# Performance work log

Measured on AMD Instinct MI355X. Metric: run time of the kernel, lower is better.

## Reference

```python
import jax, jax.numpy as jnp
import numpy as np

N_NODES = 100000
N_EDGES = 1600000
D = 64
N_GRAPHS = 64


def setup_inputs() -> dict:
    key = jax.random.key(0)
    ks = jax.random.split(key, 12)
    x = jax.random.normal(ks[0], (N_NODES, D), dtype=jnp.float32)
    edge_index = jax.random.randint(ks[1], (2, N_EDGES), 0, N_NODES, dtype=jnp.int32)
    batch = jnp.sort(jax.random.randint(ks[2], (N_NODES,), 0, N_GRAPHS, dtype=jnp.int32))
    s = 1.0 / np.sqrt(D)
    W1 = jax.random.uniform(ks[3], (D, D), jnp.float32, -s, s)
    b1 = jax.random.uniform(ks[4], (D,), jnp.float32, -s, s)
    W2 = jax.random.uniform(ks[5], (D, D), jnp.float32, -s, s)
    b2 = jax.random.uniform(ks[6], (D,), jnp.float32, -s, s)
    W3 = jax.random.uniform(ks[7], (D, D), jnp.float32, -s, s)
    b3 = jax.random.uniform(ks[8], (D,), jnp.float32, -s, s)
    lin_w = jax.random.uniform(ks[9], (D, 1), jnp.float32, -s, s)
    lin_b = jax.random.uniform(ks[10], (1,), jnp.float32, -s, s)
    return {"x": x, "edge_index": edge_index, "batch": batch,
            "W1": W1, "b1": b1, "W2": W2, "b2": b2, "W3": W3, "b3": b3,
            "lin_w": lin_w, "lin_b": lin_b}


def _gcn_conv(x, src, dst, norm, W, b):
    # PyG GCNConv: linear first, then normalized gather-scatter aggregation.
    h = x @ W                                   # [N, D]
    msg = h[src] * norm[:, None]                # [E+N, D] gathered + scaled
    out = jax.ops.segment_sum(msg, dst, num_segments=N_NODES)
    return out + b


def reference(x, edge_index, batch, W1, b1, W2, b2, W3, b3, lin_w, lin_b):
    loops = jnp.arange(N_NODES, dtype=edge_index.dtype)
    src = jnp.concatenate([edge_index[0], loops])  # source j
    dst = jnp.concatenate([edge_index[1], loops])  # target i
    # symmetric normalization D^{-1/2}(A+I)D^{-1/2}; deg >= 1 due to self loops
    deg = jax.ops.segment_sum(jnp.ones_like(dst, dtype=x.dtype), dst, num_segments=N_NODES)
    dis = jax.lax.rsqrt(deg)
    norm = dis[src] * dis[dst]                  # per-edge scalar
    h = jax.nn.relu(_gcn_conv(x, src, dst, norm, W1, b1))
    h = jax.nn.relu(_gcn_conv(h, src, dst, norm, W2, b2))
    h = jax.nn.relu(_gcn_conv(h, src, dst, norm, W3, b3))
    pooled = jax.ops.segment_sum(h, batch, num_segments=N_GRAPHS)  # global_add_pool
    return pooled @ lin_w + lin_b               # [N_GRAPHS, 1]
```

## Files before the change

kernel.cpp:

```cpp
#include <hip/hip_runtime.h>
#include <hip/hip_fp16.h>

#define D 64
#define NBMAX 512
#define BCAP 5120
#define TILE 64
#define AST 68
#define ACAP 448

typedef __attribute__((ext_vector_type(8))) short short8;
typedef __attribute__((ext_vector_type(4))) float float4v;

static __device__ __forceinline__ unsigned short f2bf(float x) {
    unsigned u = __float_as_uint(x);
    u += 0x7FFFu + ((u >> 16) & 1);
    return (unsigned short)(u >> 16);
}

__global__ void zero_ints(int* __restrict__ p, int n) {
    int i = blockIdx.x * blockDim.x + threadIdx.x;
    if (i < n) p[i] = 0;
}

__global__ void prescale_x(const float* __restrict__ x, const float* __restrict__ dis,
                           __half* __restrict__ out, int n2) {
    int i = blockIdx.x * blockDim.x + threadIdx.x;
    if (i < n2) {
        int n = i >> 5;
        float d = dis[n];
        float2 v = ((const float2*)x)[i];
        ((__half2*)out)[i] = __floats2half2_rn(v.x * d, v.y * d);
    }
}

__global__ __launch_bounds__(256) void bucket_scatter(const int* __restrict__ src,
                                                      const int* __restrict__ dst, int E,
                                                      int nb, int* __restrict__ gcursor,
                                                      unsigned* __restrict__ bpair) {
    __shared__ int lhist[NBMAX];
    __shared__ int lbase[NBMAX];
    int t = threadIdx.x;
    for (int i = t; i < nb; i += 256) lhist[i] = 0;
    __syncthreads();
    int e0 = blockIdx.x * 4096, e1 = min(e0 + 4096, E);
    for (int e = e0 + t; e < e1; e += 256) atomicAdd(&lhist[dst[e] >> 8], 1);
    __syncthreads();
    for (int i = t; i < nb; i += 256) {
        int c = lhist[i];
        lbase[i] = c ? atomicAdd(&gcursor[i], c) : 0;
        lhist[i] = 0;
    }
    __syncthreads();
    for (int e = e0 + t; e < e1; e += 256) {
        int d = dst[e];
        int b = d >> 8;
        int r = lbase[b] + atomicAdd(&lhist[b], 1);
        if (r < BCAP)
            bpair[(long)b * BCAP + r] = ((unsigned)src[e] << 8) | (unsigned)(d & 255);
    }
}

__global__ void scan_buckets(const int* __restrict__ gcursor, int B, int* __restrict__ gbase) {
    __shared__ int s[512];
    int t = threadIdx.x;
    s[t] = (t < B) ? gcursor[t] : 0;
    __syncthreads();
    for (int off = 1; off < 512; off <<= 1) {
        int v = (t >= off) ? s[t - off] : 0;
        __syncthreads();
        s[t] += v;
        __syncthreads();
    }
    if (t < B) gbase[t] = (t == 0) ? 0 : s[t - 1];
    if (t == 0) gbase[B] = s[511];
}

__global__ __launch_bounds__(256) void bucket_build(const unsigned* __restrict__ bpair,
                                                    int nb, int N,
                                                    const int* __restrict__ gcursor,
                                                    const int* __restrict__ gbase,
                                                    int* __restrict__ row_ptr,
                                                    float* __restrict__ dis,
                                                    int* __restrict__ adj) {
    __shared__ int hist[256];
    __shared__ int cur[256];
    __shared__ int wsum[4];
    int b = blockIdx.x, t = threadIdx.x;
    int cnt = gcursor[b];
    if (cnt > BCAP) cnt = BCAP;
    int ebase = gbase[b];
    const unsigned* bp = bpair + (long)b * BCAP;

    hist[t] = 0;
    __syncthreads();
    for (int i = t; i < cnt; i += 256) atomicAdd(&hist[bp[i] & 255u], 1);
    __syncthreads();
    int val = hist[t];
    int lane = t & 63, wv = t >> 6;
    int v = val;
#pragma unroll
    for (int off = 1; off < 64; off <<= 1) {
        int u = __shfl_up(v, off, 64);
        if (lane >= off) v += u;
    }
    if (lane == 63) wsum[wv] = v;
    __syncthreads();
    int wo = 0;
#pragma unroll
    for (int w = 0; w < 4; w++)
        if (w < wv) wo += wsum[w];
    int excl = wo + v - val;
    int node = (b << 8) + t;
    if (node < N) {
        row_ptr[node] = ebase + excl;
        dis[node] = rsqrtf((float)(val + 1));
    }
    cur[t] = ebase + excl;
    __syncthreads();
    for (int i = t; i < cnt; i += 256) {
        unsigned p = bp[i];
        unsigned dl = p & 255u;
        int pos = atomicAdd(&cur[dl], 1);
        adj[pos] = (int)((p >> 8) << 6) | (int)(dl & 63u);
    }
    if (b == 0 && t == 0) row_ptr[N] = gbase[nb];
}

__global__ __launch_bounds__(256) void tile_layer(const __half* __restrict__ in,
                                                  const int* __restrict__ row_ptr,
                                                  const int* __restrict__ adj,
                                                  const float* __restrict__ dis,
                                                  const float* __restrict__ Wg,
                                                  const float* __restrict__ bias,
                                                  __half* __restrict__ out,
                                                  int N, int scale_out) {
    __shared__ float acc[TILE * AST];
    __shared__ int adjbuf[4][ACAP];

    int t = threadIdx.x;
    int lane = t & 63;
    int w = t >> 6;
    int row = lane >> 2;
    int c = lane & 3;
    int c2 = c * 2;
    int col = lane & 15, quad = lane >> 4;

    int t0 = blockIdx.x * TILE;
    int wbase = t0 + w * 16;
    int node = wbase + row;

    int e0r = 0, e1r = 0;
    if (node < N) { e0r = row_ptr[node]; e1r = row_ptr[node + 1]; }

    const int4* in4 = (const int4*)in;
    int* adjw = adjbuf[w];

    float a[16];
#pragma unroll
    for (int j = 0; j < 16; j++) a[j] = 0.f;

#define ADD16(xa, ya)                                                   \
    {                                                                   \
        const __half2* h0 = (const __half2*)&(xa);                      \
        const __half2* h1 = (const __half2*)&(ya);                      \
        _Pragma("unroll")                                               \
        for (int j = 0; j < 4; j++) {                                   \
            float2 f = __half22float2(h0[j]);                           \
            a[2 * j] += f.x; a[2 * j + 1] += f.y;                       \
        }                                                               \
        _Pragma("unroll")                                               \
        for (int j = 0; j < 4; j++) {                                   \
            float2 f = __half22float2(h1[j]);                           \
            a[8 + 2 * j] += f.x; a[8 + 2 * j + 1] += f.y;               \
        }                                                               \
    }

    if (node < N) {
        long rs = (long)node * 8 + c2;
        int4 xa = in4[rs], xb = in4[rs + 1];
        ADD16(xa, xb)
    }

    int wn0 = min(wbase, N);
    int wn1 = min(wbase + 16, N);
    int eb_w = row_ptr[wn0];
    int ee_w = row_ptr[wn1];

    for (int base = eb_w; base < ee_w; base += ACAP) {
        int clen = min(ACAP, ee_w - base);
        for (int i = lane; i < clen; i += 64) adjw[i] = adj[base + i];
        __builtin_amdgcn_s_waitcnt(0);

        int ls = max(e0r - base, 0);
        int le = min(e1r - base, clen);
        int cnt = max(le - ls, 0);
        int kmax = cnt;
#pragma unroll
        for (int off = 32; off >= 1; off >>= 1) {
            int o = __shfl_xor(kmax, off, 64);
            kmax = max(kmax, o);
        }
        int sidx = min(ls, clen - 1);

        for (int k = 0; k < kmax; k += 4) {
            int i0 = ls + k;
            bool ok0 = i0 < le, ok1 = i0 + 1 < le, ok2 = i0 + 2 < le, ok3 = i0 + 3 < le;
            int p0 = adjw[ok0 ? i0 : sidx];
            int p1 = adjw[ok1 ? i0 + 1 : sidx];
            int p2 = adjw[ok2 ? i0 + 2 : sidx];
            int p3 = adjw[ok3 ? i0 + 3 : sidx];
            long r0 = (long)(p0 >> 6) * 8 + c2;
            long r1 = (long)(p1 >> 6) * 8 + c2;
            long r2 = (long)(p2 >> 6) * 8 + c2;
            long r3 = (long)(p3 >> 6) * 8 + c2;
            int4 xa0 = in4[r0], xb0 = in4[r0 + 1];
            int4 xa1 = in4[r1], xb1 = in4[r1 + 1];
            int4 xa2 = in4[r2], xb2 = in4[r2 + 1];
            int4 xa3 = in4[r3], xb3 = in4[r3 + 1];
            if (ok0) ADD16(xa0, xb0)
            if (ok1) ADD16(xa1, xb1)
            if (ok2) ADD16(xa2, xb2)
            if (ok3) ADD16(xa3, xb3)
        }
    }
#undef ADD16

    int nl = w * 16 + row;
    float* ap_out = &acc[nl * AST + c * 16];
#pragma unroll
    for (int j = 0; j < 4; j++) {
        float4v v4 = {a[4 * j], a[4 * j + 1], a[4 * j + 2], a[4 * j + 3]};
        *(float4v*)(ap_out + 4 * j) = v4;
    }
    __builtin_amdgcn_s_waitcnt(0);

    short8 Bf[2][4];
#pragma unroll
    for (int s = 0; s < 2; s++)
#pragma unroll
        for (int cc = 0; cc < 4; cc++) {
            short8 f;
#pragma unroll
            for (int j = 0; j < 8; j++)
                f[j] = (short)f2bf(Wg[(32 * s + quad * 8 + j) * D + 16 * cc + col]);
            Bf[s][cc] = f;
        }
    float bias_c[4];
#pragma unroll
    for (int cc = 0; cc < 4; cc++) bias_c[cc] = bias[16 * cc + col];

    int arow = w * 16 + col;
    int anode = t0 + arow;
    float dA = (anode < N) ? dis[anode] : 0.f;
    short8 Af[2];
#pragma unroll
    for (int s = 0; s < 2; s++) {
        const float* ap = &acc[arow * AST + 32 * s + quad * 8];
        float4v p0 = *(const float4v*)ap;
        float4v p1 = *(const float4v*)(ap + 4);
        short8 f;
#pragma unroll
        for (int j = 0; j < 4; j++) {
            f[j] = (short)f2bf(p0[j] * dA);
            f[4 + j] = (short)f2bf(p1[j] * dA);
        }
        Af[s] = f;
    }

    float4v accv[4];
#pragma unroll
    for (int cc = 0; cc < 4; cc++) {
        float4v z = {0.f, 0.f, 0.f, 0.f};
        accv[cc] = __builtin_amdgcn_mfma_f32_16x16x32_bf16(Af[0], Bf[0][cc], z, 0, 0, 0);
        accv[cc] = __builtin_amdgcn_mfma_f32_16x16x32_bf16(Af[1], Bf[1][cc], accv[cc], 0, 0, 0);
    }

#pragma unroll
    for (int r = 0; r < 4; r++) {
        int onode = t0 + w * 16 + quad * 4 + r;
        if (onode < N) {
            float dn = scale_out ? dis[onode] : 1.f;
#pragma unroll
            for (int cc = 0; cc < 4; cc++) {
                float vv = fmaxf(accv[cc][r] + bias_c[cc], 0.f) * dn;
                out[(long)onode * D + 16 * cc + col] = __float2half(vv);
            }
        }
    }
}

__global__ __launch_bounds__(256) void pool_partial(const __half* __restrict__ h,
                                                    const int* __restrict__ batch, int N,
                                                    int chunk, float* __restrict__ pooled) {
    int lane = threadIdx.x & 63;
    int wv = threadIdx.x >> 6;
    int c0 = blockIdx.x * chunk;
    int c1 = min(c0 + chunk, N);
    int g_cur = -1;
    float acc = 0.f;
    for (int n = c0 + wv; n < c1; n += 4) {
        int g = batch[n];
        if (g != g_cur) {
            if (g_cur >= 0) atomicAdd(&pooled[g_cur * D + lane], acc);
            g_cur = g;
            acc = 0.f;
        }
        acc += __half2float(h[n * D + lane]);
    }
    if (g_cur >= 0) atomicAdd(&pooled[g_cur * D + lane], acc);
}

__global__ void pool_linear(const float* __restrict__ pooled,
                            const float* __restrict__ lin_w,
                            const float* __restrict__ lin_b,
                            float* __restrict__ out, int G) {
    int lane = threadIdx.x & 63;
    int g = blockIdx.x * (blockDim.x >> 6) + (threadIdx.x >> 6);
    if (g >= G) return;
    float t = pooled[g * D + lane] * lin_w[lane];
#pragma unroll
    for (int off = 32; off >= 1; off >>= 1) t += __shfl_down(t, off, 64);
    if (lane == 0) out[g] = t + lin_b[0];
}

extern "C" void kernel_launch(void* const* d_in, const int* in_sizes, int n_in,
                              void* d_out, int out_size, void* d_ws, size_t ws_size,
                              hipStream_t stream) {
    const float* x      = (const float*)d_in[0];
    const int*   edges  = (const int*)d_in[1];
    const int*   batch  = (const int*)d_in[2];
    const float* W1     = (const float*)d_in[3];
    const float* b1     = (const float*)d_in[4];
    const float* W2     = (const float*)d_in[5];
    const float* b2     = (const float*)d_in[6];
    const float* W3     = (const float*)d_in[7];
    const float* b3     = (const float*)d_in[8];
    const float* lin_w  = (const float*)d_in[9];
    const float* lin_b  = (const float*)d_in[10];
    float* out = (float*)d_out;

    const int N = in_sizes[2];
    const int E = in_sizes[1] / 2;
    const int G = out_size;
    const int nb = (N + 255) >> 8;

    const int* e_src = edges;
    const int* e_dst = edges + E;

    auto al = [](long v) { return (v + 63) & ~63L; };
    long o_gcur   = 0;
    long o_pooled = al(o_gcur + NBMAX);
    long o_gbase  = al(o_pooled + (long)G * D);
    long o_rowptr = al(o_gbase + nb + 1);
    long o_dis    = al(o_rowptr + N + 1);
    long o_adjs   = al(o_dis + N);
    long o_xh     = al(o_adjs + E);
    long o_hA     = al(o_xh + (long)N * D / 2);
    long o_hB     = o_hA + (long)N * D;

    int*    gcursor = (int*)d_ws + o_gcur;
    float*  pooled  = (float*)d_ws + o_pooled;
    int*    gbase   = (int*)d_ws + o_gbase;
    int*    row_ptr = (int*)d_ws + o_rowptr;
    float*  dis     = (float*)d_ws + o_dis;
    int*    adj     = (int*)d_ws + o_adjs;
    __half* xh      = (__half*)((float*)d_ws + o_xh);
    __half* hA      = (__half*)((float*)d_ws + o_hA);
    __half* hB      = (__half*)((float*)d_ws + o_hB);
    unsigned* bpair = (unsigned*)hA;

    int nz = (int)(o_pooled + (long)G * D);
    zero_ints<<<(nz + 255) / 256, 256, 0, stream>>>((int*)d_ws, nz);

    bucket_scatter<<<(E + 4095) / 4096, 256, 0, stream>>>(e_src, e_dst, E, nb, gcursor, bpair);
    scan_buckets<<<1, 512, 0, stream>>>(gcursor, nb, gbase);
    bucket_build<<<nb, 256, 0, stream>>>(bpair, nb, N, gcursor, gbase, row_ptr, dis, adj);

    int n2 = N * D / 2;
    prescale_x<<<(n2 + 255) / 256, 256, 0, stream>>>(x, dis, xh, n2);

    const int tl_blocks = (N + TILE - 1) / TILE;
    tile_layer<<<tl_blocks, 256, 0, stream>>>(xh, row_ptr, adj, dis, W1, b1, hB, N, 1);
    tile_layer<<<tl_blocks, 256, 0, stream>>>(hB, row_ptr, adj, dis, W2, b2, hA, N, 1);
    tile_layer<<<tl_blocks, 256, 0, stream>>>(hA, row_ptr, adj, dis, W3, b3, hB, N, 0);

    const int pool_blocks = 512;
    const int chunk = (N + pool_blocks - 1) / pool_blocks;
    pool_partial<<<pool_blocks, 256, 0, stream>>>(hB, batch, N, chunk, pooled);
    pool_linear<<<(G + 3) / 4, 256, 0, stream>>>(pooled, lin_w, lin_b, out, G);
}
```

Before: 277.6 us.

## Shrink tile_layer registers and LDS: bf16 staging, templated gather unroll, streamed weights

Turns the GCN tile layer into a template over the gather batch size. Layer 1 keeps a 4-wide gather; layers 2 and 3 use a 2-wide gather with launch_bounds(256,8) to raise occupancy. The aggregated rows are now scaled by dis and packed to bf16 before going to LDS, which halves shared memory use. Weight fragments are loaded per column block instead of all up front, and the index math uses 32-bit byte offsets. Fewer gathers in flight per wave on layers 2 and 3 could reduce memory-level parallelism, and forcing 8 blocks per CU may cause register spills.

```diff
diff --git a/kernel.cpp b/kernel.cpp
--- a/kernel.cpp
+++ b/kernel.cpp
@@ -5,7 +5,7 @@
 #define NBMAX 512
 #define BCAP 5120
 #define TILE 64
-#define AST 68
+#define ASTH 72
 #define ACAP 448
 
 typedef __attribute__((ext_vector_type(8))) short short8;
@@ -126,15 +126,16 @@
     if (b == 0 && t == 0) row_ptr[N] = gbase[nb];
 }
 
-__global__ __launch_bounds__(256) void tile_layer(const __half* __restrict__ in,
-                                                  const int* __restrict__ row_ptr,
-                                                  const int* __restrict__ adj,
-                                                  const float* __restrict__ dis,
-                                                  const float* __restrict__ Wg,
-                                                  const float* __restrict__ bias,
-                                                  __half* __restrict__ out,
-                                                  int N, int scale_out) {
-    __shared__ float acc[TILE * AST];
+template <int NB>
+static __device__ __forceinline__ void tile_layer_body(const __half* __restrict__ in,
+                                                       const int* __restrict__ row_ptr,
+                                                       const int* __restrict__ adj,
+                                                       const float* __restrict__ dis,
+                                                       const float* __restrict__ Wg,
+                                                       const float* __restrict__ bias,
+                                                       __half* __restrict__ out,
+                                                       int N, int scale_out) {
+    __shared__ __align__(16) unsigned short accb[TILE * ASTH];
     __shared__ int adjbuf[4][ACAP];
 
     int t = threadIdx.x;
@@ -142,7 +143,6 @@
     int w = t >> 6;
     int row = lane >> 2;
     int c = lane & 3;
-    int c2 = c * 2;
     int col = lane & 15, quad = lane >> 4;
 
     int t0 = blockIdx.x * TILE;
@@ -152,8 +152,9 @@
     int e0r = 0, e1r = 0;
     if (node < N) { e0r = row_ptr[node]; e1r = row_ptr[node + 1]; }
 
-    const int4* in4 = (const int4*)in;
+    const char* inb = (const char*)in;
     int* adjw = adjbuf[w];
+    unsigned coff = (unsigned)c * 32u;
 
     float a[16];
 #pragma unroll
@@ -176,8 +177,9 @@
     }
 
     if (node < N) {
-        long rs = (long)node * 8 + c2;
-        int4 xa = in4[rs], xb = in4[rs + 1];
+        unsigned rb = (unsigned)node * 128u + coff;
+        int4 xa = *(const int4*)(inb + rb);
+        int4 xb = *(const int4*)(inb + rb + 16);
         ADD16(xa, xb)
     }
 
@@ -202,91 +204,93 @@
         }
         int sidx = min(ls, clen - 1);
 
-        for (int k = 0; k < kmax; k += 4) {
-            int i0 = ls + k;
-            bool ok0 = i0 < le, ok1 = i0 + 1 < le, ok2 = i0 + 2 < le, ok3 = i0 + 3 < le;
-            int p0 = adjw[ok0 ? i0 : sidx];
-            int p1 = adjw[ok1 ? i0 + 1 : sidx];
-            int p2 = adjw[ok2 ? i0 + 2 : sidx];
-            int p3 = adjw[ok3 ? i0 + 3 : sidx];
-            long r0 = (long)(p0 >> 6) * 8 + c2;
-            long r1 = (long)(p1 >> 6) * 8 + c2;
-            long r2 = (long)(p2 >> 6) * 8 + c2;
-            long r3 = (long)(p3 >> 6) * 8 + c2;
-            int4 xa0 = in4[r0], xb0 = in4[r0 + 1];
-            int4 xa1 = in4[r1], xb1 = in4[r1 + 1];
-            int4 xa2 = in4[r2], xb2 = in4[r2 + 1];
-            int4 xa3 = in4[r3], xb3 = in4[r3 + 1];
-            if (ok0) ADD16(xa0, xb0)
-            if (ok1) ADD16(xa1, xb1)
-            if (ok2) ADD16(xa2, xb2)
-            if (ok3) ADD16(xa3, xb3)
+        for (int k = 0; k < kmax; k += NB) {
+            bool ok[NB];
+            unsigned ro[NB];
+            int4 xa[NB], xb[NB];
+#pragma unroll
+            for (int u = 0; u < NB; u++) {
+                int idx = ls + k + u;
+                ok[u] = idx < le;
+                int pk = adjw[ok[u] ? idx : sidx];
+                ro[u] = (unsigned)(pk >> 6) * 128u + coff;
+            }
+#pragma unroll
+            for (int u = 0; u < NB; u++) {
+                xa[u] = *(const int4*)(inb + ro[u]);
+                xb[u] = *(const int4*)(inb + ro[u] + 16);
+            }
+#pragma unroll
+            for (int u = 0; u < NB; u++)
+                if (ok[u]) ADD16(xa[u], xb[u])
         }
     }
 #undef ADD16
 
-    int nl = w * 16 + row;
-    float* ap_out = &acc[nl * AST + c * 16];
-#pragma unroll
-    for (int j = 0; j < 4; j++) {
-        float4v v4 = {a[4 * j], a[4 * j + 1], a[4 * j + 2], a[4 * j + 3]};
-        *(float4v*)(ap_out + 4 * j) = v4;
-    }
+    float dA = (node < N) ? dis[node] : 0.f;
+    unsigned short* ab = &accb[(w * 16 + row) * ASTH + c * 16];
+    unsigned pk[8];
+#pragma unroll
+    for (int j = 0; j < 8; j++)
+        pk[j] = (unsigned)f2bf(a[2 * j] * dA) | ((unsigned)f2bf(a[2 * j + 1] * dA) << 16);
+    *(int4*)ab = make_int4((int)pk[0], (int)pk[1], (int)pk[2], (int)pk[3]);
+    *(int4*)(ab + 8) = make_int4((int)pk[4], (int)pk[5], (int)pk[6], (int)pk[7]);
     __builtin_amdgcn_s_waitcnt(0);
 
-    short8 Bf[2][4];
-#pragma unroll
-    for (int s = 0; s < 2; s++)
-#pragma unroll
-        for (int cc = 0; cc < 4; cc++) {
-            short8 f;
-#pragma unroll
-            for (int j = 0; j < 8; j++)
-                f[j] = (short)f2bf(Wg[(32 * s + quad * 8 + j) * D + 16 * cc + col]);
-            Bf[s][cc] = f;
-        }
-    float bias_c[4];
-#pragma unroll
-    for (int cc = 0; cc < 4; cc++) bias_c[cc] = bias[16 * cc + col];
-
-    int arow = w * 16 + col;
-    int anode = t0 + arow;
-    float dA = (anode < N) ? dis[anode] : 0.f;
-    short8 Af[2];
-#pragma unroll
-    for (int s = 0; s < 2; s++) {
-        const float* ap = &acc[arow * AST + 32 * s + quad * 8];
-        float4v p0 = *(const float4v*)ap;
-        float4v p1 = *(const float4v*)(ap + 4);
-        short8 f;
-#pragma unroll
-        for (int j = 0; j < 4; j++) {
-            f[j] = (short)f2bf(p0[j] * dA);
-            f[4 + j] = (short)f2bf(p1[j] * dA);
-        }
-        Af[s] = f;
-    }
-
-    float4v accv[4];
-#pragma unroll
-    for (int cc = 0; cc < 4; cc++) {
-        float4v z = {0.f, 0.f, 0.f, 0.f};
-        accv[cc] = __builtin_amdgcn_mfma_f32_16x16x32_bf16(Af[0], Bf[0][cc], z, 0, 0, 0);
-        accv[cc] = __builtin_amdgcn_mfma_f32_16x16x32_bf16(Af[1], Bf[1][cc], accv[cc], 0, 0, 0);
-    }
-
+    const unsigned short* arp = &accb[(w * 16 + col) * ASTH + quad * 8];
+    short8 Af0 = *(const short8*)arp;
+    short8 Af1 = *(const short8*)(arp + 32);
+
+    float dnv[4];
 #pragma unroll
     for (int r = 0; r < 4; r++) {
         int onode = t0 + w * 16 + quad * 4 + r;
-        if (onode < N) {
-            float dn = scale_out ? dis[onode] : 1.f;
-#pragma unroll
-            for (int cc = 0; cc < 4; cc++) {
-                float vv = fmaxf(accv[cc][r] + bias_c[cc], 0.f) * dn;
+        dnv[r] = (onode < N) ? (scale_out ? dis[onode] : 1.f) : 0.f;
+    }
+
+#pragma unroll
+    for (int cc = 0; cc < 4; cc++) {
+        short8 B0, B1;
+#pragma unroll
+        for (int j = 0; j < 8; j++) {
+            B0[j] = (short)f2bf(Wg[(quad * 8 + j) * D + 16 * cc + col]);
+            B1[j] = (short)f2bf(Wg[(32 + quad * 8 + j) * D + 16 * cc + col]);
+        }
+        float4v z = {0.f, 0.f, 0.f, 0.f};
+        float4v v = __builtin_amdgcn_mfma_f32_16x16x32_bf16(Af0, B0, z, 0, 0, 0);
+        v = __builtin_amdgcn_mfma_f32_16x16x32_bf16(Af1, B1, v, 0, 0, 0);
+        float bc = bias[16 * cc + col];
+#pragma unroll
+        for (int r = 0; r < 4; r++) {
+            int onode = t0 + w * 16 + quad * 4 + r;
+            if (onode < N) {
+                float vv = fmaxf(v[r] + bc, 0.f) * dnv[r];
                 out[(long)onode * D + 16 * cc + col] = __float2half(vv);
             }
         }
     }
+}
+
+__global__ __launch_bounds__(256) void tile_layer4(const __half* __restrict__ in,
+                                                   const int* __restrict__ row_ptr,
+                                                   const int* __restrict__ adj,
+                                                   const float* __restrict__ dis,
+                                                   const float* __restrict__ Wg,
+                                                   const float* __restrict__ bias,
+                                                   __half* __restrict__ out,
+                                                   int N, int scale_out) {
+    tile_layer_body<4>(in, row_ptr, adj, dis, Wg, bias, out, N, scale_out);
+}
+
+__global__ __launch_bounds__(256, 8) void tile_layer2(const __half* __restrict__ in,
+                                                      const int* __restrict__ row_ptr,
+                                                      const int* __restrict__ adj,
+                                                      const float* __restrict__ dis,
+                                                      const float* __restrict__ Wg,
+                                                      const float* __restrict__ bias,
+                                                      __half* __restrict__ out,
+                                                      int N, int scale_out) {
+    tile_layer_body<2>(in, row_ptr, adj, dis, Wg, bias, out, N, scale_out);
 }
 
 __global__ __launch_bounds__(256) void pool_partial(const __half* __restrict__ h,
@@ -380,9 +384,9 @@
     prescale_x<<<(n2 + 255) / 256, 256, 0, stream>>>(x, dis, xh, n2);
 
     const int tl_blocks = (N + TILE - 1) / TILE;
-    tile_layer<<<tl_blocks, 256, 0, stream>>>(xh, row_ptr, adj, dis, W1, b1, hB, N, 1);
-    tile_layer<<<tl_blocks, 256, 0, stream>>>(hB, row_ptr, adj, dis, W2, b2, hA, N, 1);
-    tile_layer<<<tl_blocks, 256, 0, stream>>>(hA, row_ptr, adj, dis, W3, b3, hB, N, 0);
+    tile_layer4<<<tl_blocks, 256, 0, stream>>>(xh, row_ptr, adj, dis, W1, b1, hB, N, 1);
+    tile_layer2<<<tl_blocks, 256, 0, stream>>>(hB, row_ptr, adj, dis, W2, b2, hA, N, 1);
+    tile_layer2<<<tl_blocks, 256, 0, stream>>>(hA, row_ptr, adj, dis, W3, b3, hB, N, 0);
 
     const int pool_blocks = 512;
     const int chunk = (N + pool_blocks - 1) / pool_blocks;
```

New measurement: 286.2 us. +3.1%, slower.
